# Kernel optimization log

Measured on AMD Instinct MI355X. Metric: run time of the kernel, lower is better.

The kernel has to match this reference:

```python
import jax, jax.numpy as jnp
import numpy as np

T, B = 128, 4096          # rollout length, num parallel envs
H = 128                   # lstm hidden
FEAT = 96                 # 32 (image) + 32 (loc) + 32 (energy)
NA = 6                    # num_actions
GRID, MAXE = 10.0, 200.0


def setup_inputs() -> dict:
    key = jax.random.key(0)
    ks = jax.random.split(key, 24)
    N = T * B
    w = lambda k, shp, s=0.05: (jax.random.normal(k, shp, jnp.float32) * s)
    return {
        "image": jax.random.uniform(ks[0], (N, 5, 5), jnp.float32),
        "location": jax.random.uniform(ks[1], (N, 2), jnp.float32),
        "energy": jax.random.uniform(ks[2], (N, 1), jnp.float32),
        "done": jax.random.randint(ks[3], (N,), 0, 2).astype(jnp.int32),
        "h0": jnp.zeros((B, H), jnp.float32),
        "c0": jnp.zeros((B, H), jnp.float32),
        # visual encoder MLP 25->256->256->128->32
        "W1": w(ks[4], (25, 256)),  "b1": jnp.zeros(256, jnp.float32),
        "W2": w(ks[5], (256, 256)), "b2": jnp.zeros(256, jnp.float32),
        "W3": w(ks[6], (256, 128)), "b3": jnp.zeros(128, jnp.float32),
        "W4": w(ks[7], (128, 32)),  "b4": jnp.zeros(32, jnp.float32),
        # location / energy encoders
        "Wl": w(ks[8], (2, 32)), "bl": jnp.zeros(32, jnp.float32),
        "We": w(ks[9], (1, 32)), "be": jnp.zeros(32, jnp.float32),
        # LSTM (PyTorch layout: gates [i,f,g,o], W_ih: [4H, in], W_hh: [4H, H])
        "Wih": w(ks[10], (4 * H, FEAT)), "Whh": w(ks[11], (4 * H, H)),
        "bih": jnp.zeros(4 * H, jnp.float32), "bhh": jnp.zeros(4 * H, jnp.float32),
        # actor / critic heads
        "Wa": w(ks[12], (H, NA)), "ba": jnp.zeros(NA, jnp.float32),
        "Wc": w(ks[13], (H, 1)),  "bc": jnp.zeros(1, jnp.float32),
    }


def _forward(image, location, energy, done, h0, c0,
             W1, b1, W2, b2, W3, b3, W4, b4, Wl, bl, We, be,
             Wih, Whh, bih, bhh, Wa, ba, Wc, bc):
    relu = jax.nn.relu
    x = image.reshape(-1, 25) / 255.0                      # [N,25]
    f = relu(x @ W1 + b1)
    f = relu(f @ W2 + b2)
    f = relu(f @ W3 + b3)
    img_feat = relu(f @ W4 + b4)                           # [N,32]
    loc_feat = (location / GRID) @ Wl + bl                 # [N,32]
    eng_feat = (energy / MAXE) @ We + be                   # [N,32]
    feats = jnp.concatenate([img_feat, loc_feat, eng_feat], axis=1)  # [N,96]
    xs = feats.reshape(T, B, FEAT)
    ds = done.astype(jnp.float32).reshape(T, B)
    bias = bih + bhh                                       # [4H]

    def step(carry, inp):
        h, c = carry                                       # [B,H]
        x_t, d_t = inp
        mask = (1.0 - d_t)[:, None]                        # reset on done
        h = h * mask
        c = c * mask
        gates = x_t @ Wih.T + h @ Whh.T + bias             # [B,4H]
        i, fg, g, o = jnp.split(gates, 4, axis=1)
        c = jax.nn.sigmoid(fg) * c + jax.nn.sigmoid(i) * jnp.tanh(g)
        h = jax.nn.sigmoid(o) * jnp.tanh(c)
        return (h, c), h

    (hT, cT), hs = jax.lax.scan(step, (h0, c0), (xs, ds))  # hs: [T,B,H]
    hidden = hs.reshape(-1, H)                             # [N,H]
    logits = hidden @ Wa + ba                              # [N,NA]
    value = hidden @ Wc + bc                               # [N,1]
    return jnp.concatenate([logits, value], axis=1)        # [N,NA+1]


def reference(image, location, energy, done, h0, c0,
              W1, b1, W2, b2, W3, b3, W4, b4, Wl, bl, We, be,
              Wih, Whh, bih, bhh, Wa, ba, Wc, bc):
    return _forward(image, location, energy, done, h0, c0,
                    W1, b1, W2, b2, W3, b3, W4, b4, Wl, bl, We, be,
                    Wih, Whh, bih, bhh, Wa, ba, Wc, bc)
```

## Files before the change

kernel.cpp:

```cpp
#include <hip/hip_runtime.h>

#define T_ 128
#define B_ 4096
#define N_ (T_*B_)
#define H_ 128
#define FEAT_ 96
#define K_ 224
#define G4H_ 512
#define L2E 1.4426950408889634f

typedef __attribute__((ext_vector_type(8))) short short8;
typedef __attribute__((ext_vector_type(4))) short short4v;
typedef __attribute__((ext_vector_type(4))) float f32x4;

__device__ __forceinline__ void bar_lgkm() {
    asm volatile("s_waitcnt lgkmcnt(0)\n\ts_barrier" ::: "memory");
}

__device__ __forceinline__ float sig2(float x) {
    return __builtin_amdgcn_rcpf(1.0f + __builtin_amdgcn_exp2f(-x));
}
__device__ __forceinline__ float ftanh(float x) {
    float e = __builtin_amdgcn_exp2f(-2.0f * L2E * x);
    return fmaf(2.0f, __builtin_amdgcn_rcpf(1.0f + e), -1.0f);
}
__device__ __forceinline__ short f2bf(float f) {
    unsigned u = __builtin_bit_cast(unsigned, f);
    u += 0x7fff + ((u >> 16) & 1);
    return (short)(u >> 16);
}
__device__ __forceinline__ short4v pack4relu(const f32x4 a) {
    short4v v;
    v[0] = f2bf(fmaxf(a[0], 0.f)); v[1] = f2bf(fmaxf(a[1], 0.f));
    v[2] = f2bf(fmaxf(a[2], 0.f)); v[3] = f2bf(fmaxf(a[3], 0.f));
    return v;
}

#define FBASE(t, grp, kk) ((((size_t)(t) * 256 + (grp)) * 3 + (kk)) * 512)

__global__ __launch_bounds__(256) void prep_kernel(
    const float* __restrict__ Wih, const float* __restrict__ Whh,
    const float* __restrict__ bih, const float* __restrict__ bhh,
    const float* __restrict__ W1, const float* __restrict__ W2,
    const float* __restrict__ W3, const float* __restrict__ W4,
    short* __restrict__ Wtp, float* __restrict__ bias,
    short* __restrict__ W1p, short* __restrict__ W2p,
    short* __restrict__ W3p, short* __restrict__ W4p)
{
    int idx = blockIdx.x * 256 + threadIdx.x;
    if (idx < 114688) {
        int j = idx & 7, L = (idx >> 3) & 63, r = idx >> 9;
        int kk = r % 7, n = r / 7;
        int k = kk * 32 + ((L >> 4) << 3) + j;
        int g = (n << 4) + (L & 15);
        float v = (k < FEAT_) ? Wih[g * FEAT_ + k] : Whh[g * H_ + (k - FEAT_)];
        float s = (n >= 16 && n < 24) ? (2.0f * L2E) : L2E;
        Wtp[idx] = f2bf(v * s);
        return;
    }
    int e = idx - 114688;
    if (e < 8192) {
        int j = e & 7, L = (e >> 3) & 63, nt = e >> 9;
        int k = ((L >> 4) << 3) + j;
        int o = nt * 16 + (L & 15);
        W1p[e] = (k < 25) ? f2bf(W1[k * 256 + o] * (1.0f / 255.0f)) : (short)0;
        return;
    }
    e -= 8192;
    if (e < 65536) {
        int j = e & 7, L = (e >> 3) & 63, f = e >> 9;
        int kk = f & 7, nt = f >> 3;
        int k = kk * 32 + ((L >> 4) << 3) + j;
        W2p[e] = f2bf(W2[k * 256 + nt * 16 + (L & 15)]);
        return;
    }
    e -= 65536;
    if (e < 32768) {
        int j = e & 7, L = (e >> 3) & 63, f = e >> 9;
        int kk = f & 7, nt = f >> 3;
        int k = kk * 32 + ((L >> 4) << 3) + j;
        W3p[e] = f2bf(W3[k * 128 + nt * 16 + (L & 15)]);
        return;
    }
    e -= 32768;
    if (e < 4096) {
        int j = e & 7, L = (e >> 3) & 63, f = e >> 9;
        int kk = f & 3, nt = f >> 2;
        int k = kk * 32 + ((L >> 4) << 3) + j;
        W4p[e] = f2bf(W4[k * 32 + nt * 16 + (L & 15)]);
        return;
    }
    e -= 4096;
    if (e < 512) {
        float s = ((e >> 7) == 2) ? (2.0f * L2E) : L2E;
        bias[e] = (bih[e] + bhh[e]) * s;
    }
}

__global__ __launch_bounds__(256) void loc_kernel(
    const float* __restrict__ location, const float* __restrict__ energy,
    const float* __restrict__ Wl, const float* __restrict__ bl,
    const float* __restrict__ We, const float* __restrict__ be,
    short* __restrict__ featsb)
{
    __shared__ float C[160];
    const int tid = threadIdx.x;
    if (tid < 160) {
        float v;
        if (tid < 64)       v = Wl[tid];
        else if (tid < 96)  v = bl[tid - 64];
        else if (tid < 128) v = We[tid - 96];
        else                v = be[tid - 128];
        C[tid] = v;
    }
    __syncthreads();
    const int n = blockIdx.x * 64 + (tid >> 2);
    const int p = tid & 3;
    const float lx = location[(size_t)n * 2 + 0] * 0.1f;
    const float ly = location[(size_t)n * 2 + 1] * 0.1f;
    const float ev = energy[n] * (1.0f / 200.0f);
    const int t = n >> 12, b = n & 4095;
    const int grp = b >> 4, bi = b & 15;
    const int kk = 1 + (p >> 1);
    #pragma unroll
    for (int o = 0; o < 2; o++) {
        const int f0 = 32 + p * 16 + o * 8;
        short8 v;
        #pragma unroll
        for (int j = 0; j < 8; j++) {
            const int f = f0 + j;
            float val;
            if (f < 64) { const int cix = f - 32; val = fmaf(lx, C[cix], fmaf(ly, C[32 + cix], C[64 + cix])); }
            else        { const int cix = f - 64; val = fmaf(ev, C[96 + cix], C[128 + cix]); }
            v[j] = f2bf(val);
        }
        const int Lhi = ((p & 1) << 1) + o;
        *(short8*)&featsb[FBASE(t, grp, kk) + (Lhi * 16 + bi) * 8] = v;
    }
}

__global__ __launch_bounds__(512, 2) void enc_kernel(
    const float* __restrict__ image,
    const short* __restrict__ W1p, const float* __restrict__ b1,
    const short* __restrict__ W2p, const float* __restrict__ b2,
    const short* __restrict__ W3p, const float* __restrict__ b3,
    const short* __restrict__ W4p, const float* __restrict__ b4,
    short* __restrict__ featsb)
{
    __shared__ float Raw[2][800];
    __shared__ __align__(16) short In[2 * 512];
    __shared__ __align__(16) short AA[2 * 8 * 512];
    __shared__ __align__(16) short AB[2 * 8 * 512];
    __shared__ __align__(16) short AC[2 * 4 * 512];
    const int tid  = threadIdx.x;
    const int lane = tid & 63, wv = tid >> 6;
    const int col  = lane & 15, quad = lane >> 4;

    short8 w1r[2], w2r[2][8], w3r[8], w4r[4];
    #pragma unroll
    for (int i = 0; i < 2; i++)
        w1r[i] = *(const short8*)&W1p[((wv + 8 * i) * 64 + lane) * 8];
    #pragma unroll
    for (int i = 0; i < 2; i++)
        #pragma unroll
        for (int kk = 0; kk < 8; kk++)
            w2r[i][kk] = *(const short8*)&W2p[(((wv + 8 * i) * 8 + kk) * 64 + lane) * 8];
    #pragma unroll
    for (int kk = 0; kk < 8; kk++)
        w3r[kk] = *(const short8*)&W3p[((wv * 8 + kk) * 64 + lane) * 8];
    #pragma unroll
    for (int kk = 0; kk < 4; kk++)
        w4r[kk] = *(const short8*)&W4p[(((wv & 1) * 4 + kk) * 64 + lane) * 8];
    float4 b1r[2], b2r[2];
    #pragma unroll
    for (int i = 0; i < 2; i++) {
        b1r[i] = *(const float4*)(b1 + (wv + 8 * i) * 16 + quad * 4);
        b2r[i] = *(const float4*)(b2 + (wv + 8 * i) * 16 + quad * 4);
    }
    const float4 b3r = *(const float4*)(b3 + wv * 16 + quad * 4);
    const float4 b4r = *(const float4*)(b4 + (wv & 1) * 16 + quad * 4);

    const bool ld = tid < 400;
    const int w4t = tid - 256;
    float2 ir = {0.f, 0.f};

    if (ld) {
        float2 t0 = *(const float2*)(image + (size_t)blockIdx.x * 800 + 2 * tid);
        Raw[0][2 * tid] = t0.x; Raw[0][2 * tid + 1] = t0.y;
        ir = *(const float2*)(image + (size_t)(blockIdx.x + 256) * 800 + 2 * tid);
    }
    bar_lgkm();
    if (w4t >= 0 && w4t < 128) {
        const int st = w4t >> 6, L = w4t & 63;
        const int s = st * 16 + (L & 15), kb = (L >> 4) * 8;
        short8 v;
        #pragma unroll
        for (int j = 0; j < 8; j++) {
            const int kx = kb + j;
            v[j] = (kx < 25) ? f2bf(Raw[0][s * 25 + kx]) : (short)0;
        }
        *(short8*)&In[(st * 64 + L) * 8] = v;
    }

    for (int it = 0; it < 64; it++) {
        const int nxt = (it & 1) ^ 1;
        const int tile = it * 256 + blockIdx.x;
        if (ld && it + 1 < 64) { Raw[nxt][2 * tid] = ir.x; Raw[nxt][2 * tid + 1] = ir.y; }
        if (ld && it + 2 < 64)
            ir = *(const float2*)(image + (size_t)(tile + 512) * 800 + 2 * tid);
        bar_lgkm();

        {
            short8 bx[2];
            #pragma unroll
            for (int st = 0; st < 2; st++) bx[st] = *(const short8*)&In[(st * 64 + lane) * 8];
            #pragma unroll
            for (int i = 0; i < 2; i++) {
                const int nt = wv + 8 * i;
                #pragma unroll
                for (int st = 0; st < 2; st++) {
                    f32x4 acc = (f32x4){b1r[i].x, b1r[i].y, b1r[i].z, b1r[i].w};
                    acc = __builtin_amdgcn_mfma_f32_16x16x32_bf16(w1r[i], bx[st], acc, 0, 0, 0);
                    *(short4v*)&AA[((st * 8 + (nt >> 1)) * 64 + ((((nt & 1) << 1) + (quad >> 1)) << 4) + col) * 8 + (quad & 1) * 4]
                        = pack4relu(acc);
                }
            }
        }
        bar_lgkm();

        {
            f32x4 acc[2][2];
            #pragma unroll
            for (int i = 0; i < 2; i++)
                #pragma unroll
                for (int st = 0; st < 2; st++)
                    acc[i][st] = (f32x4){b2r[i].x, b2r[i].y, b2r[i].z, b2r[i].w};
            #pragma unroll
            for (int kk = 0; kk < 8; kk++) {
                short8 bx[2];
                #pragma unroll
                for (int st = 0; st < 2; st++)
                    bx[st] = *(const short8*)&AA[((st * 8 + kk) * 64 + lane) * 8];
                #pragma unroll
                for (int i = 0; i < 2; i++)
                    #pragma unroll
                    for (int st = 0; st < 2; st++)
                        acc[i][st] = __builtin_amdgcn_mfma_f32_16x16x32_bf16(w2r[i][kk], bx[st], acc[i][st], 0, 0, 0);
            }
            #pragma unroll
            for (int i = 0; i < 2; i++) {
                const int nt = wv + 8 * i;
                #pragma unroll
                for (int st = 0; st < 2; st++)
                    *(short4v*)&AB[((st * 8 + (nt >> 1)) * 64 + ((((nt & 1) << 1) + (quad >> 1)) << 4) + col) * 8 + (quad & 1) * 4]
                        = pack4relu(acc[i][st]);
            }
        }
        bar_lgkm();

        {
            f32x4 acc[2];
            #pragma unroll
            for (int st = 0; st < 2; st++) acc[st] = (f32x4){b3r.x, b3r.y, b3r.z, b3r.w};
            #pragma unroll
            for (int kk = 0; kk < 8; kk++) {
                #pragma unroll
                for (int st = 0; st < 2; st++) {
                    const short8 bx = *(const short8*)&AB[((st * 8 + kk) * 64 + lane) * 8];
                    acc[st] = __builtin_amdgcn_mfma_f32_16x16x32_bf16(w3r[kk], bx, acc[st], 0, 0, 0);
                }
            }
            const int nt = wv;
            #pragma unroll
            for (int st = 0; st < 2; st++)
                *(short4v*)&AC[((st * 4 + (nt >> 1)) * 64 + ((((nt & 1) << 1) + (quad >> 1)) << 4) + col) * 8 + (quad & 1) * 4]
                    = pack4relu(acc[st]);
        }
        bar_lgkm();

        if (wv < 4) {
            const int nt = wv & 1, st = wv >> 1;
            f32x4 acc = (f32x4){b4r.x, b4r.y, b4r.z, b4r.w};
            #pragma unroll
            for (int kk = 0; kk < 4; kk++) {
                const short8 bx = *(const short8*)&AC[((st * 4 + kk) * 64 + lane) * 8];
                acc = __builtin_amdgcn_mfma_f32_16x16x32_bf16(w4r[kk], bx, acc, 0, 0, 0);
            }
            const int t4 = tile >> 7;
            const int grp = (tile & 127) * 2 + st;
            *(short4v*)&featsb[FBASE(t4, grp, 0) + (((nt << 1) + (quad >> 1)) * 16 + col) * 8 + (quad & 1) * 4]
                = pack4relu(acc);
        } else if (w4t >= 0 && w4t < 128 && it + 1 < 64) {
            const int st = w4t >> 6, L = w4t & 63;
            const int s = st * 16 + (L & 15), kb = (L >> 4) * 8;
            short8 v;
            #pragma unroll
            for (int j = 0; j < 8; j++) {
                const int kx = kb + j;
                v[j] = (kx < 25) ? f2bf(Raw[nxt][s * 25 + kx]) : (short)0;
            }
            *(short8*)&In[(st * 64 + L) * 8] = v;
        }
    }
}

__global__ __launch_bounds__(512, 2) void lstm_kernel(
    const short* __restrict__ featsb, const int* __restrict__ done,
    const float* __restrict__ h0, const float* __restrict__ c0,
    const short* __restrict__ Wtp, const float* __restrict__ bias,
    const float* __restrict__ Wa, const float* __restrict__ ba,
    const float* __restrict__ Wc, const float* __restrict__ bc,
    float* __restrict__ out)
{
    __shared__ __align__(16) short Hb[2][4 * 64 * 8];
    __shared__ __align__(16) short HW[4 * 64 * 8];
    __shared__ float Ml[T_ * 16];

    const int tid = threadIdx.x;
    const int r0 = blockIdx.x * 16;
    const int grp = r0 >> 4;
    const int lane = tid & 63;
    const int wv = tid >> 6;
    const int col = lane & 15;
    const int quad = lane >> 4;
    const int u = (wv << 4) + col;

    short8 wtr[4][7];
    #pragma unroll
    for (int g = 0; g < 4; g++)
        #pragma unroll
        for (int kk = 0; kk < 7; kk++)
            wtr[g][kk] = *(const short8*)&Wtp[((size_t)((wv + 8 * g) * 7 + kk) * 64 + lane) * 8];

    for (int idx = tid; idx < 4 * 64 * 8; idx += 512) {
        int j = idx & 7, L = (idx >> 3) & 63, kk2 = idx >> 9;
        int k = kk2 * 32 + ((L >> 4) << 3) + j;
        int n = L & 15;
        float v = (n < 6) ? Wa[k * 6 + n] : (n == 6 ? Wc[k] : 0.0f);
        HW[idx] = f2bf(v);
    }
    for (int idx = tid; idx < T_ * 16; idx += 512)
        Ml[idx] = 1.0f - (float)done[(size_t)(idx >> 4) * B_ + r0 + (idx & 15)];

    const int kk2h = wv >> 1;
    const int Lhi_h = ((wv & 1) << 1) | (col >> 3);
    const int jh = col & 7;
    f32x4 c;
    #pragma unroll
    for (int r = 0; r < 4; r++) {
        const int s = (quad << 2) + r;
        const float m = 1.0f - (float)done[r0 + s];
        c[r] = c0[(size_t)(r0 + s) * H_ + u] * m;
        Hb[0][(kk2h * 64 + Lhi_h * 16 + s) * 8 + jh] = f2bf(h0[(size_t)(r0 + s) * H_ + u]);
    }
    const float bi0 = bias[((wv +  0) << 4) + col];
    const float bi1 = bias[((wv +  8) << 4) + col];
    const float bi2 = bias[((wv + 16) << 4) + col];
    const float bi3 = bias[((wv + 24) << 4) + col];
    const float hb = (col < 6) ? ba[col] : (col == 6 ? bc[0] : 0.0f);

    short8 xa[3], xb[3];
    #pragma unroll
    for (int kk = 0; kk < 3; kk++) {
        xa[kk] = *(const short8*)&featsb[FBASE(0, grp, kk) + lane * 8];
        xb[kk] = *(const short8*)&featsb[FBASE(1, grp, kk) + lane * 8];
    }
    bar_lgkm();

    auto STEP = [&](int t, int cur, short8* X) {
        const int nxt = cur ^ 1;
        const float mcol = Ml[t * 16 + col];
        f32x4 acc0 = {bi0, bi0, bi0, bi0};
        f32x4 acc1 = {bi1, bi1, bi1, bi1};
        f32x4 acc2 = {bi2, bi2, bi2, bi2};
        f32x4 acc3 = {bi3, bi3, bi3, bi3};
        #pragma unroll
        for (int kk = 0; kk < 7; kk++) {
            short8 af;
            if (kk < 3) af = X[kk];
            else {
                af = *(const short8*)&Hb[cur][((kk - 3) * 64 + lane) * 8];
                if (mcol == 0.0f) af = (short8){0,0,0,0,0,0,0,0};
            }
            acc0 = __builtin_amdgcn_mfma_f32_16x16x32_bf16(af, wtr[0][kk], acc0, 0, 0, 0);
            acc1 = __builtin_amdgcn_mfma_f32_16x16x32_bf16(af, wtr[1][kk], acc1, 0, 0, 0);
            acc2 = __builtin_amdgcn_mfma_f32_16x16x32_bf16(af, wtr[2][kk], acc2, 0, 0, 0);
            acc3 = __builtin_amdgcn_mfma_f32_16x16x32_bf16(af, wtr[3][kk], acc3, 0, 0, 0);
        }
        float4 mn = {1.f, 1.f, 1.f, 1.f};
        if (t < T_ - 1) mn = *(const float4*)&Ml[(t + 1) * 16 + (quad << 2)];
        #pragma unroll
        for (int r = 0; r < 4; r++) {
            const float ig = sig2(acc0[r]);
            const float fg = sig2(acc1[r]);
            const float gt = fmaf(2.0f, sig2(acc2[r]), -1.0f);
            const float og = sig2(acc3[r]);
            const float cn = fmaf(fg, c[r], ig * gt);
            const float h = og * ftanh(cn);
            c[r] = cn * ((&mn.x)[r]);
            Hb[nxt][(kk2h * 64 + Lhi_h * 16 + (quad << 2) + r) * 8 + jh] = f2bf(h);
        }
        if (t + 2 < T_) {
            #pragma unroll
            for (int kk = 0; kk < 3; kk++)
                X[kk] = *(const short8*)&featsb[FBASE(t + 2, grp, kk) + lane * 8];
        }
        bar_lgkm();

        if (wv == (t & 7)) {
            f32x4 ha = {hb, hb, hb, hb};
            #pragma unroll
            for (int kk2 = 0; kk2 < 4; kk2++) {
                const short8 hf = *(const short8*)&Hb[nxt][(kk2 * 64 + lane) * 8];
                const short8 wf = *(const short8*)&HW[(kk2 * 64 + lane) * 8];
                ha = __builtin_amdgcn_mfma_f32_16x16x32_bf16(hf, wf, ha, 0, 0, 0);
            }
            if (col < 7) {
                #pragma unroll
                for (int r = 0; r < 4; r++) {
                    const int s = (quad << 2) + r;
                    out[((size_t)t * B_ + r0 + s) * 7 + col] = ha[r];
                }
            }
        }
    };

    for (int t = 0; t < T_; t += 2) {
        STEP(t, 0, xa);
        STEP(t + 1, 1, xb);
    }
}

extern "C" void kernel_launch(void* const* d_in, const int* in_sizes, int n_in,
                              void* d_out, int out_size, void* d_ws, size_t ws_size,
                              hipStream_t stream) {
    const float* image    = (const float*)d_in[0];
    const float* location = (const float*)d_in[1];
    const float* energy   = (const float*)d_in[2];
    const int*   done     = (const int*)d_in[3];
    const float* h0       = (const float*)d_in[4];
    const float* c0       = (const float*)d_in[5];
    const float* W1 = (const float*)d_in[6];   const float* b1 = (const float*)d_in[7];
    const float* W2 = (const float*)d_in[8];   const float* b2 = (const float*)d_in[9];
    const float* W3 = (const float*)d_in[10];  const float* b3 = (const float*)d_in[11];
    const float* W4 = (const float*)d_in[12];  const float* b4 = (const float*)d_in[13];
    const float* Wl = (const float*)d_in[14];  const float* bl = (const float*)d_in[15];
    const float* We = (const float*)d_in[16];  const float* be = (const float*)d_in[17];
    const float* Wih = (const float*)d_in[18]; const float* Whh = (const float*)d_in[19];
    const float* bih = (const float*)d_in[20]; const float* bhh = (const float*)d_in[21];
    const float* Wa = (const float*)d_in[22];  const float* ba = (const float*)d_in[23];
    const float* Wc = (const float*)d_in[24];  const float* bc = (const float*)d_in[25];

    char* ws = (char*)d_ws;
    short* Wtp   = (short*)ws;
    float* bias  = (float*)(ws + 229376);
    short* W1p   = (short*)(ws + 231424);
    short* W2p   = (short*)(ws + 247808);
    short* W3p   = (short*)(ws + 378880);
    short* W4p   = (short*)(ws + 444416);
    short* featsb = (short*)(ws + 452608);
    float* out   = (float*)d_out;

    prep_kernel<<<882, 256, 0, stream>>>(Wih, Whh, bih, bhh, W1, W2, W3, W4,
                                         Wtp, bias, W1p, W2p, W3p, W4p);
    loc_kernel<<<N_ / 64, 256, 0, stream>>>(location, energy, Wl, bl, We, be, featsb);
    enc_kernel<<<256, 512, 0, stream>>>(image, W1p, b1, W2p, b2, W3p, b3, W4p, b4, featsb);
    lstm_kernel<<<B_ / 16, 512, 0, stream>>>(featsb, done, h0, c0, Wtp, bias,
                                             Wa, ba, Wc, bc, out);
}
```

Before: 430.4 us.

## Precompute next-step input projection off the LSTM recurrent critical path

The LSTM step now seeds its gate accumulators with an input projection computed during the previous step, so only the four recurrent MFMA chunks stay on the serial dependency chain. The independent x-projection MFMAs for the next timestep are issued alongside the gate math, and feature prefetch is moved to the start of the step. Float-to-bf16 conversion now uses the hardware v_cvt_pk_bf16_f32 instruction, and launch bounds drop to one block per SIMD group to allow more registers. The extra live accumulators raise register pressure, and the lower occupancy hint could reduce latency hiding.

```diff
diff --git a/kernel.cpp b/kernel.cpp
--- a/kernel.cpp
+++ b/kernel.cpp
@@ -25,15 +25,18 @@
     return fmaf(2.0f, __builtin_amdgcn_rcpf(1.0f + e), -1.0f);
 }
 __device__ __forceinline__ short f2bf(float f) {
-    unsigned u = __builtin_bit_cast(unsigned, f);
-    u += 0x7fff + ((u >> 16) & 1);
-    return (short)(u >> 16);
+    unsigned r;
+    asm("v_cvt_pk_bf16_f32 %0, %1, %2" : "=v"(r) : "v"(f), "v"(f));
+    return (short)(r & 0xffff);
 }
 __device__ __forceinline__ short4v pack4relu(const f32x4 a) {
-    short4v v;
-    v[0] = f2bf(fmaxf(a[0], 0.f)); v[1] = f2bf(fmaxf(a[1], 0.f));
-    v[2] = f2bf(fmaxf(a[2], 0.f)); v[3] = f2bf(fmaxf(a[3], 0.f));
-    return v;
+    const float x0 = fmaxf(a[0], 0.f), x1 = fmaxf(a[1], 0.f);
+    const float x2 = fmaxf(a[2], 0.f), x3 = fmaxf(a[3], 0.f);
+    unsigned r01, r23;
+    asm("v_cvt_pk_bf16_f32 %0, %1, %2" : "=v"(r01) : "v"(x0), "v"(x1));
+    asm("v_cvt_pk_bf16_f32 %0, %1, %2" : "=v"(r23) : "v"(x2), "v"(x3));
+    uint2 u; u.x = r01; u.y = r23;
+    return __builtin_bit_cast(short4v, u);
 }
 
 #define FBASE(t, grp, kk) ((((size_t)(t) * 256 + (grp)) * 3 + (kk)) * 512)
@@ -304,7 +307,7 @@
     }
 }
 
-__global__ __launch_bounds__(512, 2) void lstm_kernel(
+__global__ __launch_bounds__(512, 1) void lstm_kernel(
     const short* __restrict__ featsb, const int* __restrict__ done,
     const float* __restrict__ h0, const float* __restrict__ c0,
     const short* __restrict__ Wtp, const float* __restrict__ bias,
@@ -365,28 +368,50 @@
         xa[kk] = *(const short8*)&featsb[FBASE(0, grp, kk) + lane * 8];
         xb[kk] = *(const short8*)&featsb[FBASE(1, grp, kk) + lane * 8];
     }
+    f32x4 axA[4], axB[4];
+    axA[0] = (f32x4){bi0, bi0, bi0, bi0};
+    axA[1] = (f32x4){bi1, bi1, bi1, bi1};
+    axA[2] = (f32x4){bi2, bi2, bi2, bi2};
+    axA[3] = (f32x4){bi3, bi3, bi3, bi3};
+    #pragma unroll
+    for (int kk = 0; kk < 3; kk++) {
+        axA[0] = __builtin_amdgcn_mfma_f32_16x16x32_bf16(xa[kk], wtr[0][kk], axA[0], 0, 0, 0);
+        axA[1] = __builtin_amdgcn_mfma_f32_16x16x32_bf16(xa[kk], wtr[1][kk], axA[1], 0, 0, 0);
+        axA[2] = __builtin_amdgcn_mfma_f32_16x16x32_bf16(xa[kk], wtr[2][kk], axA[2], 0, 0, 0);
+        axA[3] = __builtin_amdgcn_mfma_f32_16x16x32_bf16(xa[kk], wtr[3][kk], axA[3], 0, 0, 0);
+    }
     bar_lgkm();
 
-    auto STEP = [&](int t, int cur, short8* X) {
+    auto STEP = [&](int t, int cur, short8* Xload, short8* Xuse, f32x4* axT, f32x4* axN) {
         const int nxt = cur ^ 1;
+        if (t + 2 < T_) {
+            #pragma unroll
+            for (int kk = 0; kk < 3; kk++)
+                Xload[kk] = *(const short8*)&featsb[FBASE(t + 2, grp, kk) + lane * 8];
+        }
         const float mcol = Ml[t * 16 + col];
-        f32x4 acc0 = {bi0, bi0, bi0, bi0};
-        f32x4 acc1 = {bi1, bi1, bi1, bi1};
-        f32x4 acc2 = {bi2, bi2, bi2, bi2};
-        f32x4 acc3 = {bi3, bi3, bi3, bi3};
-        #pragma unroll
-        for (int kk = 0; kk < 7; kk++) {
-            short8 af;
-            if (kk < 3) af = X[kk];
-            else {
-                af = *(const short8*)&Hb[cur][((kk - 3) * 64 + lane) * 8];
-                if (mcol == 0.0f) af = (short8){0,0,0,0,0,0,0,0};
-            }
-            acc0 = __builtin_amdgcn_mfma_f32_16x16x32_bf16(af, wtr[0][kk], acc0, 0, 0, 0);
-            acc1 = __builtin_amdgcn_mfma_f32_16x16x32_bf16(af, wtr[1][kk], acc1, 0, 0, 0);
-            acc2 = __builtin_amdgcn_mfma_f32_16x16x32_bf16(af, wtr[2][kk], acc2, 0, 0, 0);
-            acc3 = __builtin_amdgcn_mfma_f32_16x16x32_bf16(af, wtr[3][kk], acc3, 0, 0, 0);
-        }
+        f32x4 acc0 = axT[0], acc1 = axT[1], acc2 = axT[2], acc3 = axT[3];
+        #pragma unroll
+        for (int kk2 = 0; kk2 < 4; kk2++) {
+            short8 af = *(const short8*)&Hb[cur][(kk2 * 64 + lane) * 8];
+            if (mcol == 0.0f) af = (short8){0,0,0,0,0,0,0,0};
+            acc0 = __builtin_amdgcn_mfma_f32_16x16x32_bf16(af, wtr[0][3 + kk2], acc0, 0, 0, 0);
+            acc1 = __builtin_amdgcn_mfma_f32_16x16x32_bf16(af, wtr[1][3 + kk2], acc1, 0, 0, 0);
+            acc2 = __builtin_amdgcn_mfma_f32_16x16x32_bf16(af, wtr[2][3 + kk2], acc2, 0, 0, 0);
+            acc3 = __builtin_amdgcn_mfma_f32_16x16x32_bf16(af, wtr[3][3 + kk2], acc3, 0, 0, 0);
+        }
+        f32x4 n0 = (f32x4){bi0, bi0, bi0, bi0};
+        f32x4 n1 = (f32x4){bi1, bi1, bi1, bi1};
+        f32x4 n2 = (f32x4){bi2, bi2, bi2, bi2};
+        f32x4 n3 = (f32x4){bi3, bi3, bi3, bi3};
+        #pragma unroll
+        for (int kk = 0; kk < 3; kk++) {
+            n0 = __builtin_amdgcn_mfma_f32_16x16x32_bf16(Xuse[kk], wtr[0][kk], n0, 0, 0, 0);
+            n1 = __builtin_amdgcn_mfma_f32_16x16x32_bf16(Xuse[kk], wtr[1][kk], n1, 0, 0, 0);
+            n2 = __builtin_amdgcn_mfma_f32_16x16x32_bf16(Xuse[kk], wtr[2][kk], n2, 0, 0, 0);
+            n3 = __builtin_amdgcn_mfma_f32_16x16x32_bf16(Xuse[kk], wtr[3][kk], n3, 0, 0, 0);
+        }
+        axN[0] = n0; axN[1] = n1; axN[2] = n2; axN[3] = n3;
         float4 mn = {1.f, 1.f, 1.f, 1.f};
         if (t < T_ - 1) mn = *(const float4*)&Ml[(t + 1) * 16 + (quad << 2)];
         #pragma unroll
@@ -400,11 +425,6 @@
             c[r] = cn * ((&mn.x)[r]);
             Hb[nxt][(kk2h * 64 + Lhi_h * 16 + (quad << 2) + r) * 8 + jh] = f2bf(h);
         }
-        if (t + 2 < T_) {
-            #pragma unroll
-            for (int kk = 0; kk < 3; kk++)
-                X[kk] = *(const short8*)&featsb[FBASE(t + 2, grp, kk) + lane * 8];
-        }
         bar_lgkm();
 
         if (wv == (t & 7)) {
@@ -426,8 +446,8 @@
     };
 
     for (int t = 0; t < T_; t += 2) {
-        STEP(t, 0, xa);
-        STEP(t + 1, 1, xb);
+        STEP(t,     0, xa, xb, axA, axB);
+        STEP(t + 1, 1, xb, xa, axB, axA);
     }
 }
 
```

Result: faster. 405.2 us (-5.9%).
